# Kernel optimization log

Hardware: AMD Instinct MI355X
Metric: run time of the kernel (lower is better)

The kernel has to match this reference:

```python
import jax, jax.numpy as jnp
import numpy as np

B, CIN, H, W = 4, 256, 128, 128
PL = 128                     # plane == width (base_width=32, groups=1)
K, PAD, STR, DIL = 3, 1, 1, 1
KK = K * K


def setup_inputs() -> dict:
    key = jax.random.key(0)
    ks = jax.random.split(key, 24)
    rn = lambda k, s, sc=1.0: jax.random.normal(k, s, jnp.float32) * sc
    un = lambda k, s: jax.random.uniform(k, s, jnp.float32, 0.5, 1.5)
    return {
        'x': rn(ks[0], (B, CIN, H, W)),
        # conv1 (1x1, bias=False) + its folded eval-mode BN (scale/shift), then the extra bn1
        'w1': rn(ks[1], (PL, CIN), 0.05),
        's1a': un(ks[2], (PL,)), 't1a': rn(ks[3], (PL,), 0.1),
        's1b': un(ks[4], (PL,)), 't1b': rn(ks[5], (PL,), 0.1),
        # ModulatedDeformConvPack: offset/mask conv (3*K*K out channels) + deform conv weight/bias
        'w_off': rn(ks[6], (3 * KK, PL, K, K), 0.01),
        'b_off': rn(ks[7], (3 * KK,), 0.01),
        'w_dc': rn(ks[8], (PL, PL, K, K), 0.05),
        'b_dc': rn(ks[9], (PL,), 0.05),
        's2': un(ks[10], (PL,)), 't2': rn(ks[11], (PL,), 0.1),
        # conv3 (1x1, bias=False) + folded BN, then extra bn3
        'w3': rn(ks[12], (PL, PL), 0.05),
        's3a': un(ks[13], (PL,)), 't3a': rn(ks[14], (PL,), 0.1),
        's3b': un(ks[15], (PL,)), 't3b': rn(ks[16], (PL,), 0.1),
        # downsample: 1x1 conv (default bias=True) + folded BN
        'w_ds': rn(ks[17], (PL, CIN), 0.05),
        'b_ds': rn(ks[18], (PL,), 0.05),
        'sd': un(ks[19], (PL,)), 'td': rn(ks[20], (PL,), 0.1),
    }


def bn(x, s, t):
    # eval-mode BatchNorm folded to per-channel affine
    return x * s[None, :, None, None] + t[None, :, None, None]


def conv1x1(x, w):
    return jnp.einsum('bchw,oc->bohw', x, w)


def conv3x3(x, w, b):
    y = jax.lax.conv_general_dilated(
        x, w, (STR, STR), [(PAD, PAD), (PAD, PAD)], rhs_dilation=(DIL, DIL),
        dimension_numbers=('NCHW', 'OIHW', 'NCHW'))
    return y + b[None, :, None, None]


def bilinear_sample(x, py, px):
    """x: [B,C,H,W]; py/px: [B,KK,Ho,Wo] absolute sampling coords.
    Zero padding outside the image (per-corner validity, as in DCNv2)."""
    Bx, C, Hx, Wx = x.shape
    y0 = jnp.floor(py)
    x0 = jnp.floor(px)
    wy = py - y0   # [B,KK,Ho,Wo]
    wx = px - x0
    y0i = y0.astype(jnp.int32)
    x0i = x0.astype(jnp.int32)

    def per_b(xb, y0b, x0b, wyb, wxb):
        xf = xb.reshape(C, Hx * Wx)
        def g(iy, ix):
            valid = ((iy >= 0) & (iy < Hx) & (ix >= 0) & (ix < Wx)).astype(xb.dtype)
            idx = (jnp.clip(iy, 0, Hx - 1) * Wx + jnp.clip(ix, 0, Wx - 1)).reshape(-1)
            return jnp.take(xf, idx, axis=1).reshape((C,) + iy.shape) * valid[None]
        v00 = g(y0b, x0b)
        v01 = g(y0b, x0b + 1)
        v10 = g(y0b + 1, x0b)
        v11 = g(y0b + 1, x0b + 1)
        return (v00 * ((1 - wyb) * (1 - wxb))[None] + v01 * ((1 - wyb) * wxb)[None]
              + v10 * (wyb * (1 - wxb))[None] + v11 * (wyb * wxb)[None])

    return jax.vmap(per_b)(x, y0i, x0i, wy, wx)   # [B,C,KK,Ho,Wo]


def reference(x, w1, s1a, t1a, s1b, t1b, w_off, b_off, w_dc, b_dc, s2, t2,
              w3, s3a, t3a, s3b, t3b, w_ds, b_ds, sd, td):
    # conv1 sequential (conv+BN+ReLU), then the redundant bn1+relu from forward()
    out = jax.nn.relu(bn(conv1x1(x, w1), s1a, t1a))
    out = jax.nn.relu(bn(out, s1b, t1b))

    # --- ModulatedDeformConvPack (DCNv2) ---
    off = conv3x3(out, w_off, b_off)              # [B,3*KK,Ho,Wo]
    o1, o2, o3 = jnp.split(off, 3, axis=1)        # dy, dx, mask logits: each [B,KK,Ho,Wo]
    mask = jax.nn.sigmoid(o3)
    Ho, Wo = o1.shape[2], o1.shape[3]
    ky = (jnp.repeat(jnp.arange(K), K) * DIL).astype(jnp.float32)   # [KK]
    kx = (jnp.tile(jnp.arange(K), K) * DIL).astype(jnp.float32)
    base_y = (jnp.arange(Ho) * STR - PAD).astype(jnp.float32)
    base_x = (jnp.arange(Wo) * STR - PAD).astype(jnp.float32)
    py = base_y[None, None, :, None] + ky[None, :, None, None] + o1  # [B,KK,Ho,Wo]
    px = base_x[None, None, None, :] + kx[None, :, None, None] + o2
    sampled = bilinear_sample(out, py, px) * mask[:, None]           # [B,C,KK,Ho,Wo]
    out = jnp.einsum('oik,bikhw->bohw', w_dc.reshape(PL, PL, KK), sampled)
    out = out + b_dc[None, :, None, None]

    out = jax.nn.relu(bn(out, s2, t2))            # bn2 + relu
    out = jax.nn.relu(bn(conv1x1(out, w3), s3a, t3a))   # conv3 sequential
    out = bn(out, s3b, t3b)                       # bn3

    ident = bn(conv1x1(x, w_ds) + b_ds[None, :, None, None], sd, td)  # downsample
    return jax.nn.relu(out + ident)
```

## Files before the change

kernel.cpp:

```cpp
#include <hip/hip_runtime.h>
#include <hip/hip_bf16.h>
#include <hip/hip_fp16.h>

#define HW 16384

typedef unsigned short u16;
typedef unsigned int   u32;
typedef __attribute__((ext_vector_type(8))) short short8v;
typedef __attribute__((ext_vector_type(8))) _Float16 half8v;
typedef __attribute__((ext_vector_type(2))) __fp16 fp16x2;
typedef __attribute__((ext_vector_type(4))) float float4v;

__device__ __forceinline__ float b2f(u16 v) { return __uint_as_float((u32)v << 16); }
__device__ __forceinline__ u16 f2bf(float f) {
  u32 u = __float_as_uint(f);
  u32 r = (u + 0x7fffu + ((u >> 16) & 1u)) >> 16;
  return (u16)r;
}
__device__ __forceinline__ u16 f2h(float f) {
  _Float16 h = (_Float16)f;
  return *(u16*)&h;
}
__device__ __forceinline__ float bflo(u32 u) { return __uint_as_float(u << 16); }
__device__ __forceinline__ float bfhi(u32 u) { return __uint_as_float(u & 0xffff0000u); }
__device__ __forceinline__ u32 pkt(float a, float b) {
  return __builtin_amdgcn_perm(__float_as_uint(b), __float_as_uint(a), 0x07060302u);
}
__device__ __forceinline__ u16 bft(float v) { return (u16)(__float_as_uint(v) >> 16); }
__device__ __forceinline__ u32 pkh(float a, float b) {
  union { fp16x2 h; u32 u; } cv;
  cv.h = __builtin_amdgcn_cvt_pkrtz(a, b);
  return cv.u;
}

__global__ __launch_bounds__(256) void k_init(const float* __restrict__ w_dc,
                                              const float* __restrict__ w1,
                                              const float* __restrict__ w_ds,
                                              const float* __restrict__ w3,
                                              const float* __restrict__ w_off,
                                              u16* __restrict__ wTb, u16* __restrict__ wB1,
                                              u16* __restrict__ w3b, u16* __restrict__ woffb) {
  int idx = blockIdx.x * 256 + threadIdx.x;
  if (idx < 147456) {
    int ntile = idx / 18432, r = idx % 18432;
    int ks = r / 512, r2 = r % 512;
    int lane = r2 / 8, j = r2 % 8;
    int o = ntile * 16 + (lane & 15);
    int k = ks * 32 + ((lane >> 4) * 8) + j;
    int tap = k >> 7, ci = k & 127;
    wTb[idx] = f2h(w_dc[(o * 128 + ci) * 9 + tap]);
  }
  int i1 = idx - 147456;
  if (i1 >= 0 && i1 < 65536) {
    int ntile = i1 / 4096, r = i1 % 4096;
    int ks = r / 512, r2 = r % 512;
    int lane = r2 / 8, j = r2 % 8;
    int o = ntile * 16 + (lane & 15);
    int c = ks * 32 + ((lane >> 4) * 8) + j;
    float v = (ntile < 8) ? w1[o * 256 + c] : w_ds[(o - 128) * 256 + c];
    wB1[i1] = f2bf(v);
  }
  int i2 = idx - 212992;
  if (i2 >= 0 && i2 < 16384) {
    int ntile = i2 / 2048, r = i2 % 2048;
    int ks = r / 512, r2 = r % 512;
    int lane = r2 / 8, j = r2 % 8;
    int o = ntile * 16 + (lane & 15);
    int c = ks * 32 + ((lane >> 4) * 8) + j;
    w3b[i2] = f2bf(w3[o * 128 + c]);
  }
  int i3 = idx - 229376;
  if (i3 >= 0 && i3 < 36864) {
    int ntile = i3 / 18432, r = i3 % 18432;
    int ks = r / 512, r2 = r % 512;
    int lane = r2 / 8, j = r2 % 8;
    int oc = ntile * 16 + (lane & 15);
    int k = ks * 32 + ((lane >> 4) * 8) + j;
    int tap = k >> 7, c = k & 127;
    woffb[i3] = (oc < 27) ? f2h(w_off[oc * 1152 + c * 9 + tap]) : (u16)0;
  }
}

__global__ __launch_bounds__(256) void k_fused1(const float* __restrict__ x,
                                                const u16* __restrict__ wB1,
                                                const float* __restrict__ s1a, const float* __restrict__ t1a,
                                                const float* __restrict__ s1b, const float* __restrict__ t1b,
                                                const float* __restrict__ b_ds,
                                                const float* __restrict__ sd, const float* __restrict__ td,
                                                u16* __restrict__ out1,
                                                u16* __restrict__ identb)
{
  __shared__ __align__(16) u16 xA[8704];
  const int tid = threadIdx.x;
  const int wq = blockIdx.x, h = blockIdx.y, b = blockIdx.z;
  const int wave = tid >> 6, lane = tid & 63;

  {
    const float* xb = x + (size_t)b * 256 * HW + h * 128 + wq * 32;
    u32* dst = (u32*)xA;
    int cp = tid >> 3, wg = tid & 7;
#pragma unroll
    for (int i = 0; i < 4; ++i) {
      int cpair = i * 32 + cp;
      int c0 = cpair * 2;
      float4 va = *(const float4*)&xb[(size_t)c0 * HW + wg * 4];
      float4 vb = *(const float4*)&xb[(size_t)(c0 + 1) * HW + wg * 4];
      int p0 = wg * 4;
      dst[(p0 + 0) * 133 + cpair] = pkt(va.x, vb.x);
      dst[(p0 + 1) * 133 + cpair] = pkt(va.y, vb.y);
      dst[(p0 + 2) * 133 + cpair] = pkt(va.z, vb.z);
      dst[(p0 + 3) * 133 + cpair] = pkt(va.w, vb.w);
    }
  }
  __syncthreads();

  const int nlo = lane & 15, kgr = lane >> 4;
  float4v acc[2][4];
#pragma unroll
  for (int mt = 0; mt < 2; ++mt)
#pragma unroll
    for (int nt = 0; nt < 4; ++nt) acc[mt][nt] = (float4v)(0.f);

  const u16* a0p = &xA[nlo * 266 + kgr * 8];
  const u16* a1p = &xA[(nlo + 16) * 266 + kgr * 8];
  const u16* bp = &wB1[(((size_t)(wave * 4) * 8) * 64 + lane) * 8];

#pragma unroll
  for (int ks = 0; ks < 8; ++ks) {
    short8v a0 = *(const short8v*)(a0p + ks * 32);
    short8v a1 = *(const short8v*)(a1p + ks * 32);
#pragma unroll
    for (int nt = 0; nt < 4; ++nt) {
      short8v bv = *(const short8v*)(bp + nt * 4096 + ks * 512);
      acc[0][nt] = __builtin_amdgcn_mfma_f32_16x16x32_bf16(a0, bv, acc[0][nt], 0, 0, 0);
      acc[1][nt] = __builtin_amdgcn_mfma_f32_16x16x32_bf16(a1, bv, acc[1][nt], 0, 0, 0);
    }
  }
  __syncthreads();

  u16* P1 = xA;
  u16* T1 = xA + 4352;

  const int rbase = kgr * 4;
  if (wave < 2) {
#pragma unroll
    for (int nt = 0; nt < 4; ++nt) {
      int o = (wave * 4 + nt) * 16 + nlo;
      float sa = s1a[o], ta = t1a[o], sb = s1b[o], tb = t1b[o];
#pragma unroll
      for (int mt = 0; mt < 2; ++mt)
#pragma unroll
        for (int r = 0; r < 4; ++r) {
          float v = acc[mt][nt][r];
          v = fmaxf(sa * v + ta, 0.f);
          v = fmaxf(sb * v + tb, 0.f);
          int pos = mt * 16 + rbase + r;
          P1[pos * 136 + o] = f2h(v);
        }
    }
  } else {
#pragma unroll
    for (int nt = 0; nt < 4; ++nt) {
      int og = (wave * 4 + nt) * 16 + nlo - 128;
      float sv = sd[og], tv = td[og], bv = b_ds[og];
#pragma unroll
      for (int mt = 0; mt < 2; ++mt)
#pragma unroll
        for (int r = 0; r < 4; ++r) {
          float v = sv * (acc[mt][nt][r] + bv) + tv;
          T1[og * 34 + mt * 16 + rbase + r] = bft(v);
        }
    }
  }
  __syncthreads();

  {
    size_t rowbase = ((size_t)((b * 128 + h) * 128 + wq * 32)) * 128;
#pragma unroll
    for (int i = 0; i < 2; ++i) {
      int s = i * 256 + tid;
      int pos = s >> 4, q = s & 15;
      uint4 v = *(const uint4*)&P1[pos * 136 + q * 8];
      *(uint4*)&out1[rowbase + (size_t)pos * 128 + q * 8] = v;
    }
  }
  {
    int o = tid >> 1, half = tid & 1;
    const u16* src = &T1[o * 34 + half * 16];
    u32 bb[8];
#pragma unroll
    for (int i = 0; i < 8; ++i) bb[i] = *(const u32*)(src + i * 2);
    size_t g = ((size_t)((b * 128 + o) * 128 + h)) * 128 + wq * 32 + half * 16;
    *(uint4*)&identb[g] = make_uint4(bb[0], bb[1], bb[2], bb[3]);
    *(uint4*)&identb[g + 8] = make_uint4(bb[4], bb[5], bb[6], bb[7]);
  }
}

__global__ __launch_bounds__(512, 4) void k_dcn(const u16* __restrict__ out1,
                                                const u16* __restrict__ wTb,
                                                const u16* __restrict__ w3b,
                                                const u16* __restrict__ woffb,
                                                const float* __restrict__ b_off,
                                                const float* __restrict__ b_dc,
                                                const float* __restrict__ s2, const float* __restrict__ t2,
                                                const float* __restrict__ s3a, const float* __restrict__ t3a,
                                                const float* __restrict__ s3b, const float* __restrict__ t3b,
                                                const u16* __restrict__ identb,
                                                float* __restrict__ out) {
  __shared__ __align__(16) u16 U[36416];

  u16*   W    = U;
  float* offp = (float*)((char*)U + 54400);
  u32*   Jl   = (u32*)((char*)U + 54400);
  float* Pp   = (float*)((char*)U + 17408);
  u16*   P    = U;
  float* T2   = (float*)((char*)U + 17408);

  const int tid = threadIdx.x;
  const int flat = blockIdx.x + (blockIdx.y << 3) + (blockIdx.z << 8);
  const int nid = (flat & 7) * 128 + (flat >> 3);
  const int wq = nid & 7, th = (nid >> 3) & 31, b = nid >> 8;
  const int h0 = th * 4, w0 = wq * 16;
  const int wave = tid >> 6, lane = tid & 63;
  const int nlo = lane & 15, kgr = lane >> 4;
  const u16* base = out1 + (size_t)b * HW * 128;

  for (int k = tid; k < 3200; k += 512) {
    int pix = k >> 4, q = k & 15;
    int ri = pix / 20, ci = pix % 20;
    int y = h0 - 2 + ri, x = w0 - 2 + ci;
    uint4 g = make_uint4(0u, 0u, 0u, 0u);
    if ((y >= 0) & (y < 128) & (x >= 0) & (x < 128))
      g = *(const uint4*)&base[((size_t)(y * 128 + x)) * 128 + q * 8];
    *(uint4*)&W[pix * 136 + q * 8] = g;
  }
  __syncthreads();

  {
    const int ntile = wave & 1, mt = wave >> 1;
    float4v oacc = (float4v)(0.f);
    for (int t = 0; t < 9; ++t) {
      int ty = t / 3, tx = t % 3;
      const u16* bp = &woffb[(((size_t)(ntile * 36 + t * 4)) * 64 + lane) * 8];
      const u16* ap = &W[((mt + ty + 1) * 20 + nlo + tx + 1) * 136 + kgr * 8];
#pragma unroll
      for (int ksl = 0; ksl < 4; ++ksl) {
        half8v bv = *(const half8v*)(bp + ksl * 512);
        half8v a = *(const half8v*)(ap + ksl * 32);
        oacc = __builtin_amdgcn_mfma_f32_16x16x32_f16(a, bv, oacc, 0, 0, 0);
      }
    }
    int oc = ntile * 16 + nlo;
#pragma unroll
    for (int r = 0; r < 4; ++r)
      offp[(mt * 16 + kgr * 4 + r) * 32 + oc] = oacc[r];
  }
  __syncthreads();

  u32  jc[2][4];
  float jw[2][4];
#pragma unroll
  for (int it = 0; it < 2; ++it) {
    int j = tid + it * 512;
    if (j < 576) {
      int pos = j / 9, tap = j % 9;
      int pr = pos >> 4, pc = pos & 15;
      int hh = h0 + pr, w = w0 + pc;
      float dy  = offp[pos * 32 + tap]      + b_off[tap];
      float dxv = offp[pos * 32 + 9 + tap]  + b_off[9 + tap];
      float sg  = offp[pos * 32 + 18 + tap] + b_off[18 + tap];
      float mk = 1.f / (1.f + __expf(-sg));
      float py = (float)(hh - 1 + tap / 3) + dy;
      float px = (float)(w - 1 + tap % 3) + dxv;
      float fy = floorf(py), fx = floorf(px);
      int y0 = (int)fy, x0 = (int)fx;
      float wy = py - fy, wxf = px - fx;
      bool vy0 = (y0 >= 0) & (y0 < 128), vy1 = (y0 >= -1) & (y0 < 127);
      bool vx0 = (x0 >= 0) & (x0 < 128), vx1 = (x0 >= -1) & (x0 < 127);
      jw[it][0] = (vy0 & vx0) ? (1.f - wy) * (1.f - wxf) * mk : 0.f;
      jw[it][1] = (vy0 & vx1) ? (1.f - wy) * wxf * mk : 0.f;
      jw[it][2] = (vy1 & vx0) ? wy * (1.f - wxf) * mk : 0.f;
      jw[it][3] = (vy1 & vx1) ? wy * wxf * mk : 0.f;
      int y0c = min(max(y0, 0), 127), y1c = min(max(y0 + 1, 0), 127);
      int x0c = min(max(x0, 0), 127), x1c = min(max(x0 + 1, 0), 127);
      auto enc = [&](int yc, int xc) -> u32 {
        int ri = yc - (h0 - 2), ci = xc - (w0 - 2);
        if (((unsigned)ri < 10u) && ((unsigned)ci < 20u))
          return 0x80000000u | (u32)((ri * 20 + ci) * 136);
        return (u32)((yc * 128 + xc) * 128);
      };
      jc[it][0] = enc(y0c, x0c);
      jc[it][1] = enc(y0c, x1c);
      jc[it][2] = enc(y1c, x0c);
      jc[it][3] = enc(y1c, x1c);
    }
  }
  __syncthreads();
#pragma unroll
  for (int it = 0; it < 2; ++it) {
    int j = tid + it * 512;
    if (j < 576) {
      u32* jt = &Jl[j * 8];
      jt[0] = jc[it][0]; jt[1] = jc[it][1]; jt[2] = jc[it][2]; jt[3] = jc[it][3];
      ((float*)jt)[4] = jw[it][0]; ((float*)jt)[5] = jw[it][1];
      ((float*)jt)[6] = jw[it][2]; ((float*)jt)[7] = jw[it][3];
    }
  }
  __syncthreads();

  float4v acc8[2][8];
#pragma unroll
  for (int ms = 0; ms < 2; ++ms)
#pragma unroll
    for (int nt = 0; nt < 8; ++nt) acc8[ms][nt] = (float4v)(0.f);
  {
    const int ks = wave & 3, mh = wave >> 2;
    const int ch0 = ks * 32 + kgr * 8;
    const int jrowA = (mh * 32 + nlo) * 9;
    const int jrowB = jrowA + 144;

    auto BLD = [&](int jidx) -> half8v {
      const u32* jt = &Jl[jidx * 8];
      uint4 co4 = *(const uint4*)jt;
      float4 w4 = *(const float4*)(jt + 4);
      u32 cos[4] = {co4.x, co4.y, co4.z, co4.w};
      float wf[4] = {w4.x, w4.y, w4.z, w4.w};
      float alo[4] = {0.f, 0.f, 0.f, 0.f};
      float ahi[4] = {0.f, 0.f, 0.f, 0.f};
#pragma unroll
      for (int c = 0; c < 4; ++c) {
        u32 co = cos[c];
        short8v cv;
        if (co & 0x80000000u)
          cv = *(const short8v*)&W[(co & 0x7fffffffu) + ch0];
        else
          cv = *(const short8v*)(base + co + ch0);
        union { short8v s; _Float16 h[8]; } cc; cc.s = cv;
        float wk = wf[c];
#pragma unroll
        for (int p = 0; p < 4; ++p) {
          alo[p] = fmaf(wk, (float)cc.h[2 * p],     alo[p]);
          ahi[p] = fmaf(wk, (float)cc.h[2 * p + 1], ahi[p]);
        }
      }
      union { u32 u[4]; half8v s; } av;
#pragma unroll
      for (int p = 0; p < 4; ++p) av.u[p] = pkh(alo[p], ahi[p]);
      return av.s;
    };

#pragma unroll
    for (int t = 0; t < 9; ++t) {
      half8v av0 = BLD(jrowA + t);
      half8v av1 = BLD(jrowB + t);
      const u16* bb = &wTb[(((size_t)(t * 4 + ks)) * 64 + lane) * 8];
      __builtin_amdgcn_s_setprio(1);
#pragma unroll
      for (int nt = 0; nt < 8; ++nt) {
        half8v bv = *(const half8v*)(bb + (size_t)nt * 18432);
        acc8[0][nt] = __builtin_amdgcn_mfma_f32_16x16x32_f16(av0, bv, acc8[0][nt], 0, 0, 0);
        acc8[1][nt] = __builtin_amdgcn_mfma_f32_16x16x32_f16(av1, bv, acc8[1][nt], 0, 0, 0);
      }
      __builtin_amdgcn_s_setprio(0);
    }
  }
  __syncthreads();

  {
    const int ks = wave & 3, mh = wave >> 2;
#pragma unroll
    for (int s = 0; s < 4; ++s) {
      const int smh = s >> 1, sms = s & 1;
      if (mh == smh) {
#pragma unroll
        for (int nt = 0; nt < 8; ++nt)
#pragma unroll
          for (int r = 0; r < 4; ++r)
            Pp[ks * 2048 + (kgr * 4 + r) * 128 + nt * 16 + nlo] = acc8[sms][nt][r];
      }
      __syncthreads();
#pragma unroll
      for (int q = 0; q < 4; ++q) {
        int idx = q * 512 + tid;
        int p16 = idx >> 7, o = idx & 127;
        const float* Pb = Pp + p16 * 128 + o;
        float sum = Pb[0] + Pb[2048] + Pb[4096] + Pb[6144];
        float v = sum + b_dc[o];
        v = fmaxf(s2[o] * v + t2[o], 0.f);
        P[(s * 16 + p16) * 136 + o] = bft(v);
      }
      __syncthreads();
    }
  }

  float4v acc2[4];
#pragma unroll
  for (int mt = 0; mt < 4; ++mt) acc2[mt] = (float4v)(0.f);
  {
    const u16* bp3 = &w3b[(((size_t)(wave * 4)) * 64 + lane) * 8];
#pragma unroll
    for (int ks3 = 0; ks3 < 4; ++ks3) {
      short8v bv = *(const short8v*)(bp3 + ks3 * 512);
#pragma unroll
      for (int mt = 0; mt < 4; ++mt) {
        short8v a = *(const short8v*)&P[(mt * 16 + nlo) * 136 + ks3 * 32 + kgr * 8];
        acc2[mt] = __builtin_amdgcn_mfma_f32_16x16x32_bf16(a, bv, acc2[mt], 0, 0, 0);
      }
    }
  }

  {
    int o = wave * 16 + nlo;
    float sa = s3a[o], ta = t3a[o], sb = s3b[o], tb = t3b[o];
#pragma unroll
    for (int mt = 0; mt < 4; ++mt)
#pragma unroll
      for (int r = 0; r < 4; ++r) {
        float v = acc2[mt][r];
        v = fmaxf(sa * v + ta, 0.f);
        v = sb * v + tb;
        T2[o * 65 + mt * 16 + kgr * 4 + r] = v;
      }
  }
  __syncthreads();

  {
    int o = tid >> 2, qd = tid & 3;
    size_t g = ((size_t)((b * 128 + o) * 128 + h0 + qd)) * 128 + w0;
    const float* trow = &T2[o * 65 + qd * 16];
    uint4 iv0 = *(const uint4*)&identb[g];
    uint4 iv1 = *(const uint4*)&identb[g + 8];
    u32 iw[8] = {iv0.x, iv0.y, iv0.z, iv0.w, iv1.x, iv1.y, iv1.z, iv1.w};
#pragma unroll
    for (int q = 0; q < 4; ++q) {
      float r0 = trow[q * 4 + 0] + bflo(iw[q * 2]);
      float r1 = trow[q * 4 + 1] + bfhi(iw[q * 2]);
      float r2 = trow[q * 4 + 2] + bflo(iw[q * 2 + 1]);
      float r3 = trow[q * 4 + 3] + bfhi(iw[q * 2 + 1]);
      float4 ov = make_float4(fmaxf(r0, 0.f), fmaxf(r1, 0.f), fmaxf(r2, 0.f), fmaxf(r3, 0.f));
      *(float4*)&out[g + q * 4] = ov;
    }
  }
}

extern "C" void kernel_launch(void* const* d_in, const int* in_sizes, int n_in,
                              void* d_out, int out_size, void* d_ws, size_t ws_size,
                              hipStream_t stream) {
  const float* x     = (const float*)d_in[0];
  const float* w1    = (const float*)d_in[1];
  const float* s1a   = (const float*)d_in[2];
  const float* t1a   = (const float*)d_in[3];
  const float* s1b   = (const float*)d_in[4];
  const float* t1b   = (const float*)d_in[5];
  const float* w_off = (const float*)d_in[6];
  const float* b_off = (const float*)d_in[7];
  const float* w_dc  = (const float*)d_in[8];
  const float* b_dc  = (const float*)d_in[9];
  const float* s2    = (const float*)d_in[10];
  const float* t2    = (const float*)d_in[11];
  const float* w3    = (const float*)d_in[12];
  const float* s3a   = (const float*)d_in[13];
  const float* t3a   = (const float*)d_in[14];
  const float* s3b   = (const float*)d_in[15];
  const float* t3b   = (const float*)d_in[16];
  const float* w_ds  = (const float*)d_in[17];
  const float* b_ds  = (const float*)d_in[18];
  const float* sd    = (const float*)d_in[19];
  const float* td    = (const float*)d_in[20];

  char* ws = (char*)d_ws;
  u16* wTb    = (u16*)(ws + 0);
  u16* wB1    = (u16*)(ws + 294912);
  u16* w3b    = (u16*)(ws + 425984);
  u16* woffb  = (u16*)(ws + 458752);
  u16* out1   = (u16*)(ws + 532480);
  u16* identb = (u16*)(ws + 17309696);

  k_init  <<<1040, 256, 0, stream>>>(w_dc, w1, w_ds, w3, w_off, wTb, wB1, w3b, woffb);
  k_fused1<<<dim3(4, 128, 4), 256, 0, stream>>>(x, wB1, s1a, t1a, s1b, t1b, b_ds, sd, td, out1, identb);
  k_dcn   <<<dim3(8, 32, 4), 512, 0, stream>>>(out1, wTb, w3b, woffb, b_off, b_dc, s2, t2,
                                               s3a, t3a, s3b, t3b, identb, (float*)d_out);
}
```

Measured before the change: 227.2 us.

## Double DCN tile height to eight rows per block for more weight reuse

The deformable-conv kernel now processes an 8x16 pixel tile per block instead of 4x16, halving the grid. Each wave holds four M-subtiles of accumulators so every loaded weight fragment feeds twice as many MFMAs, and the halo staging shrinks relative to output. The block now needs more LDS and registers, so the occupancy hint drops from 4 to 2 blocks per CU. With only 512 blocks this also risks weaker latency hiding and a less even load across CUs.

```diff
diff --git a/kernel.cpp b/kernel.cpp
--- a/kernel.cpp
+++ b/kernel.cpp
@@ -196,7 +196,7 @@
   }
 }
 
-__global__ __launch_bounds__(512, 4) void k_dcn(const u16* __restrict__ out1,
+__global__ __launch_bounds__(512, 2) void k_dcn(const u16* __restrict__ out1,
                                                 const u16* __restrict__ wTb,
                                                 const u16* __restrict__ w3b,
                                                 const u16* __restrict__ woffb,
@@ -207,25 +207,25 @@
                                                 const float* __restrict__ s3b, const float* __restrict__ t3b,
                                                 const u16* __restrict__ identb,
                                                 float* __restrict__ out) {
-  __shared__ __align__(16) u16 U[36416];
+  __shared__ __align__(16) u16 U[51072];
 
   u16*   W    = U;
-  float* offp = (float*)((char*)U + 54400);
-  u32*   Jl   = (u32*)((char*)U + 54400);
-  float* Pp   = (float*)((char*)U + 17408);
+  float* offp = (float*)((char*)U + 65280);
+  u32*   Jl   = (u32*)((char*)U + 65280);
+  float* Pp   = (float*)((char*)U + 34816);
   u16*   P    = U;
-  float* T2   = (float*)((char*)U + 17408);
+  float* T2   = (float*)((char*)U + 34816);
 
   const int tid = threadIdx.x;
-  const int flat = blockIdx.x + (blockIdx.y << 3) + (blockIdx.z << 8);
-  const int nid = (flat & 7) * 128 + (flat >> 3);
-  const int wq = nid & 7, th = (nid >> 3) & 31, b = nid >> 8;
-  const int h0 = th * 4, w0 = wq * 16;
+  const int flat = blockIdx.x + (blockIdx.y << 3) + (blockIdx.z << 7);
+  const int nid = (flat & 7) * 64 + (flat >> 3);
+  const int wq = nid & 7, th = (nid >> 3) & 15, b = nid >> 7;
+  const int h0 = th * 8, w0 = wq * 16;
   const int wave = tid >> 6, lane = tid & 63;
   const int nlo = lane & 15, kgr = lane >> 4;
   const u16* base = out1 + (size_t)b * HW * 128;
 
-  for (int k = tid; k < 3200; k += 512) {
+  for (int k = tid; k < 3840; k += 512) {
     int pix = k >> 4, q = k & 15;
     int ri = pix / 20, ci = pix % 20;
     int y = h0 - 2 + ri, x = w0 - 2 + ci;
@@ -237,32 +237,39 @@
   __syncthreads();
 
   {
-    const int ntile = wave & 1, mt = wave >> 1;
-    float4v oacc = (float4v)(0.f);
+    const int ntile = wave & 1, mtg = wave >> 1;
+    float4v oacc[2];
+    oacc[0] = (float4v)(0.f); oacc[1] = (float4v)(0.f);
     for (int t = 0; t < 9; ++t) {
       int ty = t / 3, tx = t % 3;
       const u16* bp = &woffb[(((size_t)(ntile * 36 + t * 4)) * 64 + lane) * 8];
-      const u16* ap = &W[((mt + ty + 1) * 20 + nlo + tx + 1) * 136 + kgr * 8];
 #pragma unroll
       for (int ksl = 0; ksl < 4; ++ksl) {
         half8v bv = *(const half8v*)(bp + ksl * 512);
-        half8v a = *(const half8v*)(ap + ksl * 32);
-        oacc = __builtin_amdgcn_mfma_f32_16x16x32_f16(a, bv, oacc, 0, 0, 0);
+#pragma unroll
+        for (int sub = 0; sub < 2; ++sub) {
+          int mt = mtg * 2 + sub;
+          const u16* ap = &W[((mt + ty + 1) * 20 + nlo + tx + 1) * 136 + ksl * 32 + kgr * 8];
+          half8v a = *(const half8v*)ap;
+          oacc[sub] = __builtin_amdgcn_mfma_f32_16x16x32_f16(a, bv, oacc[sub], 0, 0, 0);
+        }
       }
     }
     int oc = ntile * 16 + nlo;
 #pragma unroll
-    for (int r = 0; r < 4; ++r)
-      offp[(mt * 16 + kgr * 4 + r) * 32 + oc] = oacc[r];
-  }
-  __syncthreads();
-
-  u32  jc[2][4];
-  float jw[2][4];
-#pragma unroll
-  for (int it = 0; it < 2; ++it) {
+    for (int sub = 0; sub < 2; ++sub)
+#pragma unroll
+      for (int r = 0; r < 4; ++r)
+        offp[((mtg * 2 + sub) * 16 + kgr * 4 + r) * 32 + oc] = oacc[sub][r];
+  }
+  __syncthreads();
+
+  u32  jc[3][4];
+  float jw[3][4];
+#pragma unroll
+  for (int it = 0; it < 3; ++it) {
     int j = tid + it * 512;
-    if (j < 576) {
+    if (j < 1152) {
       int pos = j / 9, tap = j % 9;
       int pr = pos >> 4, pc = pos & 15;
       int hh = h0 + pr, w = w0 + pc;
@@ -285,7 +292,7 @@
       int x0c = min(max(x0, 0), 127), x1c = min(max(x0 + 1, 0), 127);
       auto enc = [&](int yc, int xc) -> u32 {
         int ri = yc - (h0 - 2), ci = xc - (w0 - 2);
-        if (((unsigned)ri < 10u) && ((unsigned)ci < 20u))
+        if (((unsigned)ri < 12u) && ((unsigned)ci < 20u))
           return 0x80000000u | (u32)((ri * 20 + ci) * 136);
         return (u32)((yc * 128 + xc) * 128);
       };
@@ -297,9 +304,9 @@
   }
   __syncthreads();
 #pragma unroll
-  for (int it = 0; it < 2; ++it) {
+  for (int it = 0; it < 3; ++it) {
     int j = tid + it * 512;
-    if (j < 576) {
+    if (j < 1152) {
       u32* jt = &Jl[j * 8];
       jt[0] = jc[it][0]; jt[1] = jc[it][1]; jt[2] = jc[it][2]; jt[3] = jc[it][3];
       ((float*)jt)[4] = jw[it][0]; ((float*)jt)[5] = jw[it][1];
@@ -308,16 +315,14 @@
   }
   __syncthreads();
 
-  float4v acc8[2][8];
-#pragma unroll
-  for (int ms = 0; ms < 2; ++ms)
+  float4v acc8[4][8];
+#pragma unroll
+  for (int ms = 0; ms < 4; ++ms)
 #pragma unroll
     for (int nt = 0; nt < 8; ++nt) acc8[ms][nt] = (float4v)(0.f);
   {
     const int ks = wave & 3, mh = wave >> 2;
     const int ch0 = ks * 32 + kgr * 8;
-    const int jrowA = (mh * 32 + nlo) * 9;
-    const int jrowB = jrowA + 144;
 
     auto BLD = [&](int jidx) -> half8v {
       const u32* jt = &Jl[jidx * 8];
@@ -351,8 +356,10 @@
 
 #pragma unroll
     for (int t = 0; t < 9; ++t) {
-      half8v av0 = BLD(jrowA + t);
-      half8v av1 = BLD(jrowB + t);
+      half8v av0 = BLD(((mh * 64 +  0) + nlo) * 9 + t);
+      half8v av1 = BLD(((mh * 64 + 16) + nlo) * 9 + t);
+      half8v av2 = BLD(((mh * 64 + 32) + nlo) * 9 + t);
+      half8v av3 = BLD(((mh * 64 + 48) + nlo) * 9 + t);
       const u16* bb = &wTb[(((size_t)(t * 4 + ks)) * 64 + lane) * 8];
       __builtin_amdgcn_s_setprio(1);
 #pragma unroll
@@ -360,6 +367,8 @@
         half8v bv = *(const half8v*)(bb + (size_t)nt * 18432);
         acc8[0][nt] = __builtin_amdgcn_mfma_f32_16x16x32_f16(av0, bv, acc8[0][nt], 0, 0, 0);
         acc8[1][nt] = __builtin_amdgcn_mfma_f32_16x16x32_f16(av1, bv, acc8[1][nt], 0, 0, 0);
+        acc8[2][nt] = __builtin_amdgcn_mfma_f32_16x16x32_f16(av2, bv, acc8[2][nt], 0, 0, 0);
+        acc8[3][nt] = __builtin_amdgcn_mfma_f32_16x16x32_f16(av3, bv, acc8[3][nt], 0, 0, 0);
       }
       __builtin_amdgcn_s_setprio(0);
     }
@@ -370,39 +379,42 @@
     const int ks = wave & 3, mh = wave >> 2;
 #pragma unroll
     for (int s = 0; s < 4; ++s) {
-      const int smh = s >> 1, sms = s & 1;
+      const int smh = s >> 1, sbase = (s & 1) * 2;
       if (mh == smh) {
 #pragma unroll
-        for (int nt = 0; nt < 8; ++nt)
-#pragma unroll
-          for (int r = 0; r < 4; ++r)
-            Pp[ks * 2048 + (kgr * 4 + r) * 128 + nt * 16 + nlo] = acc8[sms][nt][r];
+        for (int msl = 0; msl < 2; ++msl)
+#pragma unroll
+          for (int nt = 0; nt < 8; ++nt)
+#pragma unroll
+            for (int r = 0; r < 4; ++r)
+              Pp[ks * 4096 + (msl * 16 + kgr * 4 + r) * 128 + nt * 16 + nlo]
+                = acc8[sbase + msl][nt][r];
       }
       __syncthreads();
 #pragma unroll
-      for (int q = 0; q < 4; ++q) {
+      for (int q = 0; q < 8; ++q) {
         int idx = q * 512 + tid;
-        int p16 = idx >> 7, o = idx & 127;
-        const float* Pb = Pp + p16 * 128 + o;
-        float sum = Pb[0] + Pb[2048] + Pb[4096] + Pb[6144];
+        int p = idx >> 7, o = idx & 127;
+        const float* Pb = Pp + p * 128 + o;
+        float sum = Pb[0] + Pb[4096] + Pb[8192] + Pb[12288];
         float v = sum + b_dc[o];
         v = fmaxf(s2[o] * v + t2[o], 0.f);
-        P[(s * 16 + p16) * 136 + o] = bft(v);
+        P[(s * 32 + p) * 136 + o] = bft(v);
       }
       __syncthreads();
     }
   }
 
-  float4v acc2[4];
-#pragma unroll
-  for (int mt = 0; mt < 4; ++mt) acc2[mt] = (float4v)(0.f);
+  float4v acc2[8];
+#pragma unroll
+  for (int mt = 0; mt < 8; ++mt) acc2[mt] = (float4v)(0.f);
   {
     const u16* bp3 = &w3b[(((size_t)(wave * 4)) * 64 + lane) * 8];
 #pragma unroll
     for (int ks3 = 0; ks3 < 4; ++ks3) {
       short8v bv = *(const short8v*)(bp3 + ks3 * 512);
 #pragma unroll
-      for (int mt = 0; mt < 4; ++mt) {
+      for (int mt = 0; mt < 8; ++mt) {
         short8v a = *(const short8v*)&P[(mt * 16 + nlo) * 136 + ks3 * 32 + kgr * 8];
         acc2[mt] = __builtin_amdgcn_mfma_f32_16x16x32_bf16(a, bv, acc2[mt], 0, 0, 0);
       }
@@ -413,32 +425,36 @@
     int o = wave * 16 + nlo;
     float sa = s3a[o], ta = t3a[o], sb = s3b[o], tb = t3b[o];
 #pragma unroll
-    for (int mt = 0; mt < 4; ++mt)
+    for (int mt = 0; mt < 8; ++mt)
 #pragma unroll
       for (int r = 0; r < 4; ++r) {
         float v = acc2[mt][r];
         v = fmaxf(sa * v + ta, 0.f);
         v = sb * v + tb;
-        T2[o * 65 + mt * 16 + kgr * 4 + r] = v;
+        T2[o * 129 + mt * 16 + kgr * 4 + r] = v;
       }
   }
   __syncthreads();
 
   {
     int o = tid >> 2, qd = tid & 3;
-    size_t g = ((size_t)((b * 128 + o) * 128 + h0 + qd)) * 128 + w0;
-    const float* trow = &T2[o * 65 + qd * 16];
-    uint4 iv0 = *(const uint4*)&identb[g];
-    uint4 iv1 = *(const uint4*)&identb[g + 8];
-    u32 iw[8] = {iv0.x, iv0.y, iv0.z, iv0.w, iv1.x, iv1.y, iv1.z, iv1.w};
-#pragma unroll
-    for (int q = 0; q < 4; ++q) {
-      float r0 = trow[q * 4 + 0] + bflo(iw[q * 2]);
-      float r1 = trow[q * 4 + 1] + bfhi(iw[q * 2]);
-      float r2 = trow[q * 4 + 2] + bflo(iw[q * 2 + 1]);
-      float r3 = trow[q * 4 + 3] + bfhi(iw[q * 2 + 1]);
-      float4 ov = make_float4(fmaxf(r0, 0.f), fmaxf(r1, 0.f), fmaxf(r2, 0.f), fmaxf(r3, 0.f));
-      *(float4*)&out[g + q * 4] = ov;
+#pragma unroll
+    for (int rr = 0; rr < 2; ++rr) {
+      int row = qd * 2 + rr;
+      size_t g = ((size_t)((b * 128 + o) * 128 + h0 + row)) * 128 + w0;
+      const float* trow = &T2[o * 129 + row * 16];
+      uint4 iv0 = *(const uint4*)&identb[g];
+      uint4 iv1 = *(const uint4*)&identb[g + 8];
+      u32 iw[8] = {iv0.x, iv0.y, iv0.z, iv0.w, iv1.x, iv1.y, iv1.z, iv1.w};
+#pragma unroll
+      for (int q = 0; q < 4; ++q) {
+        float r0 = trow[q * 4 + 0] + bflo(iw[q * 2]);
+        float r1 = trow[q * 4 + 1] + bfhi(iw[q * 2]);
+        float r2 = trow[q * 4 + 2] + bflo(iw[q * 2 + 1]);
+        float r3 = trow[q * 4 + 3] + bfhi(iw[q * 2 + 1]);
+        float4 ov = make_float4(fmaxf(r0, 0.f), fmaxf(r1, 0.f), fmaxf(r2, 0.f), fmaxf(r3, 0.f));
+        *(float4*)&out[g + q * 4] = ov;
+      }
     }
   }
 }
@@ -478,6 +494,6 @@
 
   k_init  <<<1040, 256, 0, stream>>>(w_dc, w1, w_ds, w3, w_off, wTb, wB1, w3b, woffb);
   k_fused1<<<dim3(4, 128, 4), 256, 0, stream>>>(x, wB1, s1a, t1a, s1b, t1b, b_ds, sd, td, out1, identb);
-  k_dcn   <<<dim3(8, 32, 4), 512, 0, stream>>>(out1, wTb, w3b, woffb, b_off, b_dc, s2, t2,
+  k_dcn   <<<dim3(8, 16, 4), 512, 0, stream>>>(out1, wTb, w3b, woffb, b_off, b_dc, s2, t2,
                                                s3a, t3a, s3b, t3b, identb, (float*)d_out);
 }
```

New measurement: 233.0 us. 1.03x slower.
